# Performance work log

Measured on AMD Instinct MI355X. Metric: run time of the kernel, lower is better.

Reference implementation:

```python
import jax, jax.numpy as jnp
import numpy as np

N = 100000      # nodes
E = 1600000     # edges (avg degree 16)
F_IN = 128      # num_features
H = 128         # hidden_channels
OUT = 64        # out_channels


def _glorot(key, shape):
    lim = float(np.sqrt(6.0 / (shape[0] + shape[1])))
    return jax.random.uniform(key, shape, jnp.float32, -lim, lim)


def setup_inputs() -> dict:
    key = jax.random.key(0)
    ks = jax.random.split(key, 5)
    x = jax.random.normal(ks[0], (N, F_IN), jnp.float32)
    edge_index = jax.random.randint(ks[1], (2, E), 0, N, dtype=jnp.int64)
    W1 = _glorot(ks[2], (F_IN, H)); b1 = jnp.zeros((H,), jnp.float32)
    W2 = _glorot(ks[3], (H, H));    b2 = jnp.zeros((H,), jnp.float32)
    W3 = _glorot(ks[4], (H, OUT));  b3 = jnp.zeros((OUT,), jnp.float32)
    return {"x": x, "edge_index": edge_index,
            "W1": W1, "b1": b1, "W2": W2, "b2": b2, "W3": W3, "b3": b3}


def _gcn_conv(h, src, dst, norm, W, b, n):
    # PyG GCNConv: linear transform, then sym-normalized scatter aggregation, then bias
    h = h @ W                                   # [N, d_out]
    msg = h[src] * norm[:, None]                # gather + scale, [E+N, d_out]
    agg = jax.ops.segment_sum(msg, dst, num_segments=n)
    return agg + b


def reference(x, edge_index, W1, b1, W2, b2, W3, b3):
    n = x.shape[0]
    # add self-loops (GCNConv default add_self_loops=True)
    loop = jnp.arange(n, dtype=edge_index.dtype)
    src = jnp.concatenate([edge_index[0], loop])
    dst = jnp.concatenate([edge_index[1], loop])
    # symmetric normalization deg^-1/2[src] * deg^-1/2[dst]
    deg = jax.ops.segment_sum(jnp.ones_like(dst, x.dtype), dst, num_segments=n)
    dinv = jnp.where(deg > 0, jax.lax.rsqrt(deg), 0.0)
    norm = dinv[src] * dinv[dst]

    h = jax.nn.relu(_gcn_conv(x, src, dst, norm, W1, b1, n))  # dropout p=0 -> no-op
    h = jax.nn.relu(_gcn_conv(h, src, dst, norm, W2, b2, n))
    h = _gcn_conv(h, src, dst, norm, W3, b3, n)
    return jax.nn.log_softmax(h, axis=1)
```

## Files before the change

kernel.cpp:

```cpp
#include <hip/hip_runtime.h>
#include <stdint.h>
#include <math.h>

#define FIN 128

typedef __attribute__((ext_vector_type(8))) short short8v;
typedef __attribute__((ext_vector_type(4))) float float4v;
typedef __attribute__((ext_vector_type(2))) float float2v;

__device__ __forceinline__ uint32_t f2_to_bf2(float x, float y) {
    uint32_t r;
    asm("v_cvt_pk_bf16_f32 %0, %1, %2" : "=v"(r) : "v"(x), "v"(y));
    return r;
}
__device__ __forceinline__ unsigned short f_to_bf(float x) {
    union { float f; uint32_t i; } a;
    a.f = x;
    uint32_t u = a.i + 0x7FFF + ((a.i >> 16) & 1);
    return (unsigned short)(u >> 16);
}
__device__ __forceinline__ void acc16_fp8_pk(float2v* acc2, uint4 v) {
    uint32_t us[4] = {v.x, v.y, v.z, v.w};
#pragma unroll
    for (int q = 0; q < 4; ++q) {
        acc2[q * 2 + 0] += __builtin_amdgcn_cvt_pk_f32_fp8(us[q], false);
        acc2[q * 2 + 1] += __builtin_amdgcn_cvt_pk_f32_fp8(us[q], true);
    }
}

template <int CTRL>
__device__ __forceinline__ float dppmov(float x) {
    int i = __builtin_bit_cast(int, x);
    int r = __builtin_amdgcn_update_dpp(i, i, CTRL, 0xF, 0xF, false);
    return __builtin_bit_cast(float, r);
}
__device__ __forceinline__ float swz16f(float x) {
    int r = __builtin_amdgcn_ds_swizzle(__builtin_bit_cast(int, x), 0x401F);
    return __builtin_bit_cast(float, r);
}

__device__ __forceinline__ int edge_at(const void* ei, long long idx, int is32) {
    return is32 ? ((const int*)ei)[idx] : (int)((const long long*)ei)[idx];
}

#define SP_CHUNK 4096
__global__ __launch_bounds__(256) void splitA_kernel(
        const void* __restrict__ ei, int* __restrict__ gCnt,
        uint32_t* __restrict__ buf1, int E, int capS, int nA,
        const float* __restrict__ W1, const float* __restrict__ W2,
        const float* __restrict__ W3, unsigned short* __restrict__ Wf1,
        unsigned short* __restrict__ Wf2, unsigned short* __restrict__ Wf3) {
    __shared__ int hist[16];
    __shared__ int gbase[16];
    __shared__ int lflag;
    int t = threadIdx.x;
    if (blockIdx.x >= nA) {
        int idx = (blockIdx.x - nA) * 256 + t;
        const float* W;
        unsigned short* Wf;
        int NCOL, base;
        if (idx < 2048)      { W = W1; Wf = Wf1; NCOL = 128; base = idx; }
        else if (idx < 4096) { W = W2; Wf = Wf2; NCOL = 128; base = idx - 2048; }
        else if (idx < 5120) { W = W3; Wf = Wf3; NCOL = 64;  base = idx - 4096; }
        else return;
        int f = base >> 6, l = base & 63;
        int ct = f >> 2, ks = f & 3;
        int nn = ct * 16 + (l & 15);
        int k0 = ks * 32 + (l >> 4) * 8;
        uint32_t pk[4];
#pragma unroll
        for (int j = 0; j < 4; ++j) {
            float a = W[(size_t)(k0 + 2 * j) * NCOL + nn];
            float b = W[(size_t)(k0 + 2 * j + 1) * NCOL + nn];
            pk[j] = f2_to_bf2(a, b);
        }
        ((uint4*)Wf)[base] = make_uint4(pk[0], pk[1], pk[2], pk[3]);
        return;
    }
    if (t < 16) hist[t] = 0;
    if (t == 0) lflag = 0;
    long long base = (long long)blockIdx.x * SP_CHUNK;
    __syncthreads();
    {
        long long e = base + t;
        if (e < E && ((const int*)ei)[2 * e + 1] != 0) atomicOr(&lflag, 1);
    }
    __syncthreads();
    int is32 = lflag;
    uint32_t lrec[16], rec[16];
#pragma unroll
    for (int j = 0; j < 16; ++j) {
        long long e = base + t + j * 256;
        if (e < E) {
            int s = edge_at(ei, e, is32);
            int d = edge_at(ei, (long long)E + e, is32);
            int b = d >> 13;
            int lofs = atomicAdd(&hist[b], 1);
            lrec[j] = ((uint32_t)lofs << 4) | (uint32_t)b;
            rec[j] = ((uint32_t)s << 13) | (uint32_t)(d & 8191);
        } else
            lrec[j] = 0xFFFFFFFFu;
    }
    __syncthreads();
    if (t < 16) gbase[t] = atomicAdd(&gCnt[t], hist[t]);
    __syncthreads();
#pragma unroll
    for (int j = 0; j < 16; ++j) {
        if (lrec[j] != 0xFFFFFFFFu) {
            int b = lrec[j] & 15;
            int pos = gbase[b] + (int)(lrec[j] >> 4);
            if (pos < capS) buf1[(size_t)b * capS + pos] = rec[j];
        }
    }
}

__global__ __launch_bounds__(256) void splitB_kernel(const int* __restrict__ gCnt,
                                                     const uint32_t* __restrict__ buf1,
                                                     int* __restrict__ cnt2,
                                                     uint32_t* __restrict__ buf2,
                                                     int capS, int cap2, int NB) {
    __shared__ int hist[128];
    __shared__ int sbase[128];
    __shared__ int gbase[128];
    __shared__ uint32_t ordrec[SP_CHUNK];
    __shared__ unsigned char ordsub[SP_CHUNK];
    int t = threadIdx.x;
    int s = blockIdx.y;
    if (t < 128) hist[t] = 0;
    __syncthreads();
    int m = gCnt[s];
    if (m > capS) m = capS;
    long long base = (long long)blockIdx.x * SP_CHUNK;
    uint32_t lrec[16], r32[16];
#pragma unroll
    for (int j = 0; j < 16; ++j) {
        long long i = base + t + j * 256;
        if (i < m) {
            uint32_t r = buf1[(size_t)s * capS + i];
            int d13 = (int)(r & 8191u);
            int sub = d13 >> 6;
            int lofs = atomicAdd(&hist[sub], 1);
            lrec[j] = ((uint32_t)lofs << 7) | (uint32_t)sub;
            r32[j] = ((r >> 13) << 6) | (uint32_t)(d13 & 63);
        } else
            lrec[j] = 0xFFFFFFFFu;
    }
    __syncthreads();
    if (t < 128) sbase[t] = hist[t];
    __syncthreads();
    for (int off = 1; off < 128; off <<= 1) {
        int v = 0;
        if (t < 128 && t >= off) v = sbase[t - off];
        __syncthreads();
        if (t < 128) sbase[t] += v;
        __syncthreads();
    }
    if (t < 128) {
        int g = s * 128 + t;
        gbase[t] = (g < NB && hist[t] > 0) ? atomicAdd(&cnt2[g], hist[t]) : 0;
        sbase[t] -= hist[t];
    }
    __syncthreads();
#pragma unroll
    for (int j = 0; j < 16; ++j) {
        if (lrec[j] != 0xFFFFFFFFu) {
            int sub = lrec[j] & 127;
            int pos = sbase[sub] + (int)(lrec[j] >> 7);
            ordrec[pos] = r32[j];
            ordsub[pos] = (unsigned char)sub;
        }
    }
    __syncthreads();
    int mloc = (int)(m - base);
    if (mloc > SP_CHUNK) mloc = SP_CHUNK;
    if (mloc < 0) mloc = 0;
    for (int i = t; i < mloc; i += 256) {
        int sub = ordsub[i];
        int gpos = gbase[sub] + (i - sbase[sub]);
        if (gpos < cap2) buf2[(size_t)(s * 128 + sub) * cap2 + gpos] = ordrec[i];
    }
}

__global__ __launch_bounds__(256) void binBC_kernel(const int* __restrict__ cnt2,
                                                    const uint32_t* __restrict__ buf2,
                                                    int* __restrict__ cnt,
                                                    float* __restrict__ dinv,
                                                    int* __restrict__ rowstart,
                                                    int* __restrict__ col,
                                                    int n, int cap2) {
    __shared__ int h[64];
    __shared__ int rowst[64];
    __shared__ int cur[64];
    __shared__ int sc[64];
    int bin = blockIdx.x;
    int t = threadIdx.x;
    if (t < 64) {
        h[t] = (bin * 64 + t < n) ? 1 : 0;
        cur[t] = 1;
    }
    __syncthreads();
    int m = cnt2[bin];
    if (m > cap2) m = cap2;
    const uint32_t* buf = buf2 + (size_t)bin * cap2;
    for (int i = t; i < m; i += 256) atomicAdd(&h[buf[i] & 63], 1);
    __syncthreads();
    int c = 0, pc = 0;
    if (t < 64) { c = h[t]; pc = (c + 7) & ~7; sc[t] = pc; }
    __syncthreads();
    for (int off = 1; off < 64; off <<= 1) {
        int v = 0;
        if (t < 64 && t >= off) v = sc[t - off];
        __syncthreads();
        if (t < 64) sc[t] += v;
        __syncthreads();
    }
    if (t < 64) {
        int node = bin * 64 + t;
        int base = bin * cap2;
        int st = base + sc[t] - pc;
        rowst[t] = st;
        if (node < n) {
            cnt[node] = c;
            dinv[node] = rsqrtf((float)c);
            rowstart[node] = st;
            col[st] = node;
            for (int k = c; k < pc; ++k) col[st + k] = n;
        }
    }
    __syncthreads();
    for (int i = t; i < m; i += 256) {
        uint32_t rec = buf[i];
        int d6 = rec & 63;
        int off = atomicAdd(&cur[d6], 1);
        col[rowst[d6] + off] = (int)(rec >> 6);
    }
}

template <int NCOL, int A_FP32, int OUT_FP8>
__global__ __launch_bounds__(256) void gemm_mfma(const void* __restrict__ Av,
                                                 const unsigned short* __restrict__ Wf,
                                                 const float* __restrict__ dinv,
                                                 void* __restrict__ Cv, int n) {
    __shared__ unsigned short lds[NCOL * 128];
    const int t = threadIdx.x;
    if (blockIdx.x == 0 && t < NCOL / 4)
        ((uint32_t*)Cv)[(size_t)n * (NCOL / 4) + t] = 0;
    for (int i = t; i < NCOL * 16; i += 256)
        ((uint4*)lds)[i] = ((const uint4*)Wf)[i];
    __syncthreads();

    const int wave = t >> 6, lane = t & 63;
    const int row0 = blockIdx.x * 64 + wave * 16;
    const int m = lane & 15, quad = lane >> 4;
    int arow = row0 + m;
    if (arow >= n) arow = n - 1;

    short8v a[4];
    if (A_FP32) {
        const float* A = (const float*)Av;
#pragma unroll
        for (int ks = 0; ks < 4; ++ks) {
            float4 lo = *(const float4*)(A + (size_t)arow * 128 + ks * 32 + quad * 8);
            float4 hi = *(const float4*)(A + (size_t)arow * 128 + ks * 32 + quad * 8 + 4);
            union { short8v v; uint32_t u[4]; } pk;
            pk.u[0] = f2_to_bf2(lo.x, lo.y);
            pk.u[1] = f2_to_bf2(lo.z, lo.w);
            pk.u[2] = f2_to_bf2(hi.x, hi.y);
            pk.u[3] = f2_to_bf2(hi.z, hi.w);
            a[ks] = pk.v;
        }
    } else {
        const unsigned short* A = (const unsigned short*)Av;
#pragma unroll
        for (int ks = 0; ks < 4; ++ks)
            a[ks] = *(const short8v*)(A + (size_t)arow * 128 + ks * 32 + quad * 8);
    }

    const int cr0 = row0 + quad * 4;
    float ds[4];
#pragma unroll
    for (int r = 0; r < 4; ++r) {
        int gr = cr0 + r;
        ds[r] = (gr < n) ? dinv[gr] : 0.0f;
    }
#pragma unroll
    for (int ct = 0; ct < NCOL / 16; ++ct) {
        float4v acc = {0.0f, 0.0f, 0.0f, 0.0f};
#pragma unroll
        for (int ks = 0; ks < 4; ++ks) {
            int f = ct * 4 + ks;
            short8v b = *(const short8v*)(lds + ((size_t)(f * 64 + lane)) * 8);
            acc = __builtin_amdgcn_mfma_f32_16x16x32_bf16(a[ks], b, acc, 0, 0, 0);
        }
#pragma unroll
        for (int r = 0; r < 4; ++r) {
            int gr = cr0 + r;
            if (gr < n) {
                float val = acc[r] * ds[r];
                if (OUT_FP8) {
                    int u = __builtin_amdgcn_cvt_pk_fp8_f32(val, val, 0, false);
                    ((unsigned char*)Cv)[(size_t)gr * NCOL + ct * 16 + m] =
                        (unsigned char)(u & 0xFF);
                } else {
                    ((unsigned short*)Cv)[(size_t)gr * NCOL + ct * 16 + m] = f_to_bf(val);
                }
            }
        }
    }
}

__global__ __launch_bounds__(256) void agg_relu_128_fp8(
        const uint32_t* __restrict__ T8, const int* __restrict__ rowstart,
        const int* __restrict__ cnt, const int* __restrict__ col,
        const float* __restrict__ dinv, const float* __restrict__ bias,
        uint32_t* __restrict__ outHb, int n) {
    int wid = blockIdx.x * 4 + (threadIdx.x >> 6);
    int lane = threadIdx.x & 63;
    int j = lane & 7, slot = (lane >> 3) & 3, sel = lane >> 5;
    int nodeA = wid * 2;
    int node = nodeA + sel;
    if (nodeA >= n) return;
    bool valid = node < n;
    int nd = valid ? node : nodeA;
    int start = rowstart[nd];
    int c = cnt[nd];
    int nit = valid ? (((c + 7) & ~7) >> 3) : 0;

    float2v acc2[8];
#pragma unroll
    for (int k = 0; k < 8; ++k) acc2[k] = (float2v){0.0f, 0.0f};
    const uint4* T4 = (const uint4*)T8;
    int bp = start + slot;
    int s00 = col[bp +  0], s01 = col[bp +  4];
    int s10 = col[bp +  8], s11 = col[bp + 12];
    int s20 = col[bp + 16], s21 = col[bp + 20];
    int s30 = col[bp + 24], s31 = col[bp + 28];
    s00 = (0 < nit) ? s00 : n;  s01 = (0 < nit) ? s01 : n;
    s10 = (1 < nit) ? s10 : n;  s11 = (1 < nit) ? s11 : n;
    s20 = (2 < nit) ? s20 : n;  s21 = (2 < nit) ? s21 : n;
    s30 = (3 < nit) ? s30 : n;  s31 = (3 < nit) ? s31 : n;
    uint4 v00 = T4[(size_t)s00 * 8 + j], v01 = T4[(size_t)s01 * 8 + j];
    uint4 v10 = T4[(size_t)s10 * 8 + j], v11 = T4[(size_t)s11 * 8 + j];
    uint4 v20 = T4[(size_t)s20 * 8 + j], v21 = T4[(size_t)s21 * 8 + j];
    uint4 v30 = T4[(size_t)s30 * 8 + j], v31 = T4[(size_t)s31 * 8 + j];
    acc16_fp8_pk(acc2, v00); acc16_fp8_pk(acc2, v01);
    acc16_fp8_pk(acc2, v10); acc16_fp8_pk(acc2, v11);
    acc16_fp8_pk(acc2, v20); acc16_fp8_pk(acc2, v21);
    acc16_fp8_pk(acc2, v30); acc16_fp8_pk(acc2, v31);
    for (int s = 4; s < nit; ++s) {
        int a0 = col[bp + s * 8], a1 = col[bp + s * 8 + 4];
        uint4 w0 = T4[(size_t)a0 * 8 + j];
        uint4 w1 = T4[(size_t)a1 * 8 + j];
        acc16_fp8_pk(acc2, w0);
        acc16_fp8_pk(acc2, w1);
    }
    float* acc = (float*)acc2;
#pragma unroll
    for (int k = 0; k < 16; ++k) acc[k] += dppmov<0x128>(acc[k]);
#pragma unroll
    for (int k = 0; k < 16; ++k) acc[k] += swz16f(acc[k]);
    if (slot == 0 && valid) {
        float di = dinv[node];
        const float4* b4 = (const float4*)bias;
        float r[16];
#pragma unroll
        for (int q = 0; q < 4; ++q) {
            float4 bb = b4[j * 4 + q];
            r[q * 4 + 0] = fmaxf(di * acc[q * 4 + 0] + bb.x, 0.0f);
            r[q * 4 + 1] = fmaxf(di * acc[q * 4 + 1] + bb.y, 0.0f);
            r[q * 4 + 2] = fmaxf(di * acc[q * 4 + 2] + bb.z, 0.0f);
            r[q * 4 + 3] = fmaxf(di * acc[q * 4 + 3] + bb.w, 0.0f);
        }
        uint4 o0, o1;
        o0.x = f2_to_bf2(r[0], r[1]);   o0.y = f2_to_bf2(r[2], r[3]);
        o0.z = f2_to_bf2(r[4], r[5]);   o0.w = f2_to_bf2(r[6], r[7]);
        o1.x = f2_to_bf2(r[8], r[9]);   o1.y = f2_to_bf2(r[10], r[11]);
        o1.z = f2_to_bf2(r[12], r[13]); o1.w = f2_to_bf2(r[14], r[15]);
        *(uint4*)(outHb + (size_t)node * 64 + j * 8) = o0;
        *(uint4*)(outHb + (size_t)node * 64 + j * 8 + 4) = o1;
    }
}

__global__ __launch_bounds__(256) void agg_lsm_64_fp8(
        const uint32_t* __restrict__ T8, const int* __restrict__ rowstart,
        const int* __restrict__ cnt, const int* __restrict__ col,
        const float* __restrict__ dinv, const float* __restrict__ bias,
        float* __restrict__ out, int n) {
    int wid = blockIdx.x * 4 + (threadIdx.x >> 6);
    int lane = threadIdx.x & 63;
    int j = lane & 3, slot = (lane >> 2) & 7, sel = lane >> 5;
    int nodeA = wid * 2;
    int node = nodeA + sel;
    if (nodeA >= n) return;
    bool valid = node < n;
    int nd = valid ? node : nodeA;
    int start = rowstart[nd];
    int c = cnt[nd];
    int nit = valid ? (((c + 7) & ~7) >> 3) : 0;

    float2v acc2[8];
#pragma unroll
    for (int k = 0; k < 8; ++k) acc2[k] = (float2v){0.0f, 0.0f};
    const uint4* T4 = (const uint4*)T8;
    int bp = start + slot;
    int a0 = col[bp +  0];
    int a1 = col[bp +  8];
    int a2 = col[bp + 16];
    int a3 = col[bp + 24];
    a0 = (0 < nit) ? a0 : n;
    a1 = (1 < nit) ? a1 : n;
    a2 = (2 < nit) ? a2 : n;
    a3 = (3 < nit) ? a3 : n;
    uint4 v0 = T4[(size_t)a0 * 4 + j];
    uint4 v1 = T4[(size_t)a1 * 4 + j];
    uint4 v2 = T4[(size_t)a2 * 4 + j];
    uint4 v3 = T4[(size_t)a3 * 4 + j];
    acc16_fp8_pk(acc2, v0);
    acc16_fp8_pk(acc2, v1);
    acc16_fp8_pk(acc2, v2);
    acc16_fp8_pk(acc2, v3);
    for (int s = 4; s < nit; ++s) {
        int aa = col[bp + s * 8];
        uint4 w = T4[(size_t)aa * 4 + j];
        acc16_fp8_pk(acc2, w);
    }
    float* acc = (float*)acc2;
#pragma unroll
    for (int k = 0; k < 16; ++k) acc[k] += dppmov<0x124>(acc[k]);
#pragma unroll
    for (int k = 0; k < 16; ++k) acc[k] += dppmov<0x128>(acc[k]);
#pragma unroll
    for (int k = 0; k < 16; ++k) acc[k] += swz16f(acc[k]);
    float di = dinv[nd];
    const float4* b4 = (const float4*)bias;
    float r[16];
#pragma unroll
    for (int q = 0; q < 4; ++q) {
        float4 bb = b4[j * 4 + q];
        r[q * 4 + 0] = di * acc[q * 4 + 0] + bb.x;
        r[q * 4 + 1] = di * acc[q * 4 + 1] + bb.y;
        r[q * 4 + 2] = di * acc[q * 4 + 2] + bb.z;
        r[q * 4 + 3] = di * acc[q * 4 + 3] + bb.w;
    }
    float m0 = fmaxf(fmaxf(r[0], r[1]), fmaxf(r[2], r[3]));
    float m1 = fmaxf(fmaxf(r[4], r[5]), fmaxf(r[6], r[7]));
    float m2 = fmaxf(fmaxf(r[8], r[9]), fmaxf(r[10], r[11]));
    float m3 = fmaxf(fmaxf(r[12], r[13]), fmaxf(r[14], r[15]));
    float m = fmaxf(fmaxf(m0, m1), fmaxf(m2, m3));
    m = fmaxf(m, dppmov<0xB1>(m));
    m = fmaxf(m, dppmov<0x4E>(m));
    float e0 = __expf(r[0] - m) + __expf(r[1] - m) + __expf(r[2] - m) +
               __expf(r[3] - m);
    float e1 = __expf(r[4] - m) + __expf(r[5] - m) + __expf(r[6] - m) +
               __expf(r[7] - m);
    float e2 = __expf(r[8] - m) + __expf(r[9] - m) + __expf(r[10] - m) +
               __expf(r[11] - m);
    float e3 = __expf(r[12] - m) + __expf(r[13] - m) + __expf(r[14] - m) +
               __expf(r[15] - m);
    float ss = (e0 + e1) + (e2 + e3);
    ss += dppmov<0xB1>(ss);
    ss += dppmov<0x4E>(ss);
    float lg = m + __logf(ss);
    if (slot == 0 && valid) {
#pragma unroll
        for (int q = 0; q < 4; ++q) {
            float4 o = make_float4(r[q * 4 + 0] - lg, r[q * 4 + 1] - lg,
                                   r[q * 4 + 2] - lg, r[q * 4 + 3] - lg);
            *(float4*)(out + (size_t)node * 64 + j * 16 + q * 4) = o;
        }
    }
}

extern "C" void kernel_launch(void* const* d_in, const int* in_sizes, int n_in,
                              void* d_out, int out_size, void* d_ws, size_t ws_size,
                              hipStream_t stream) {
    const float* x  = (const float*)d_in[0];
    const void*  ei = d_in[1];
    const float* W1 = (const float*)d_in[2];
    const float* b1 = (const float*)d_in[3];
    const float* W2 = (const float*)d_in[4];
    const float* b2 = (const float*)d_in[5];
    const float* W3 = (const float*)d_in[6];
    const float* b3 = (const float*)d_in[7];
    float* out = (float*)d_out;

    const int n = in_sizes[0] / FIN;
    const int E = in_sizes[1] / 2;

    char* p = (char*)d_ws;
    auto carve = [&](size_t bytes) {
        char* q = p;
        p += (bytes + 255) & ~(size_t)255;
        return q;
    };
    const int NB = (n + 63) / 64;
    const int NS = (n + 8191) / 8192;

    long long meanS = (long long)E * 8192 / n;
    int capS = (int)(meanS + 8 * (long long)sqrt((double)meanS) + 1024);
    capS = (capS + 15) & ~15;
    long long mean2 = (long long)E * 64 / n;
    int cap2 = (int)(mean2 + 8 * (long long)sqrt((double)mean2) + 1152);
    cap2 = (cap2 + 15) & ~15;

    int*   cnt      = (int*)carve((size_t)n * 4);
    int*   rowstart = (int*)carve((size_t)n * 4);
    float* dinv     = (float*)carve((size_t)n * 4);
    int*   colb     = (int*)carve(((size_t)NB * cap2 + 4096) * 4);
    int*   gCnt     = (int*)carve((size_t)(16 + NB) * 4);
    int*   cnt2     = gCnt + 16;
    size_t Tbytes = (size_t)n * 128 + 256;
    size_t Hbytes = (size_t)n * 128 * 2;
    char*  TH = carve(Tbytes + Hbytes);
    void*  T  = (void*)TH;
    unsigned short* Hb = (unsigned short*)(TH + Tbytes);
    unsigned short* Wf1 = (unsigned short*)carve(128 * 128 * 2);
    unsigned short* Wf2 = (unsigned short*)carve(128 * 128 * 2);
    unsigned short* Wf3 = (unsigned short*)carve(128 * 64 * 2);

    size_t buf1B = ((size_t)NS * capS * 4 + 255) & ~(size_t)255;
    uint32_t* buf1 = (uint32_t*)TH;
    uint32_t* buf2 = (uint32_t*)(TH + buf1B);
    size_t avail2 = (Tbytes + Hbytes > buf1B) ? (Tbytes + Hbytes - buf1B) : 0;
    size_t maxc2 = avail2 / ((size_t)NB * 4);
    if ((size_t)cap2 > maxc2) cap2 = (int)maxc2;

    hipMemsetAsync(gCnt, 0, (size_t)(16 + NB) * 4, stream);

    const int gagg2 = ((n + 1) / 2 + 3) / 4;
    const int ggemm = (n + 63) / 64;
    const int gsplitA = (E + SP_CHUNK - 1) / SP_CHUNK;
    const int gsplitBx = (capS + SP_CHUNK - 1) / SP_CHUNK;

    splitA_kernel<<<gsplitA + 20, 256, 0, stream>>>(ei, gCnt, buf1, E, capS, gsplitA,
                                                    W1, W2, W3, Wf1, Wf2, Wf3);
    splitB_kernel<<<dim3(gsplitBx, NS), 256, 0, stream>>>(gCnt, buf1, cnt2, buf2, capS,
                                                          cap2, NB);
    binBC_kernel<<<NB, 256, 0, stream>>>(cnt2, buf2, cnt, dinv, rowstart, colb, n,
                                         cap2);

    gemm_mfma<128, 1, 1><<<ggemm, 256, 0, stream>>>(x, Wf1, dinv, T, n);
    agg_relu_128_fp8<<<gagg2, 256, 0, stream>>>((const uint32_t*)T, rowstart, cnt,
                                                colb, dinv, b1, (uint32_t*)Hb, n);
    gemm_mfma<128, 0, 1><<<ggemm, 256, 0, stream>>>(Hb, Wf2, dinv, T, n);
    agg_relu_128_fp8<<<gagg2, 256, 0, stream>>>((const uint32_t*)T, rowstart, cnt,
                                                colb, dinv, b2, (uint32_t*)Hb, n);
    gemm_mfma<64, 0, 1><<<ggemm, 256, 0, stream>>>(Hb, Wf3, dinv, T, n);
    agg_lsm_64_fp8<<<gagg2, 256, 0, stream>>>((const uint32_t*)T, rowstart, cnt, colb,
                                              dinv, b3, out, n);
}
```

Measured before the change: 278.3 us.

## Split 128-wide aggregation into four feature slices processed by separate blocks

The 128-feature FP8 aggregation kernel now splits each node's feature row into four 32-byte slices. Blocks are interleaved so neighbouring blocks handle different slices of the same node pairs, and each lane gathers 8 bytes instead of 16. The lane layout moves to 4 feature lanes by 8 edge slots, with an extra DPP reduction step. The aim is to shrink the working set per wave and raise memory-level parallelism. The cost is four times as many blocks, each re-reading col indices and rowstart/cnt, plus smaller gather transactions.

```diff
diff --git a/kernel.cpp b/kernel.cpp
--- a/kernel.cpp
+++ b/kernel.cpp
@@ -26,6 +26,12 @@
         acc2[q * 2 + 0] += __builtin_amdgcn_cvt_pk_f32_fp8(us[q], false);
         acc2[q * 2 + 1] += __builtin_amdgcn_cvt_pk_f32_fp8(us[q], true);
     }
+}
+__device__ __forceinline__ void acc8_fp8_pk(float2v* acc2, uint2 v) {
+    acc2[0] += __builtin_amdgcn_cvt_pk_f32_fp8(v.x, false);
+    acc2[1] += __builtin_amdgcn_cvt_pk_f32_fp8(v.x, true);
+    acc2[2] += __builtin_amdgcn_cvt_pk_f32_fp8(v.y, false);
+    acc2[3] += __builtin_amdgcn_cvt_pk_f32_fp8(v.y, true);
 }
 
 template <int CTRL>
@@ -314,9 +320,12 @@
         const int* __restrict__ cnt, const int* __restrict__ col,
         const float* __restrict__ dinv, const float* __restrict__ bias,
         uint32_t* __restrict__ outHb, int n) {
-    int wid = blockIdx.x * 4 + (threadIdx.x >> 6);
+    int b = blockIdx.x;
+    int slice = (b >> 1) & 3;
+    int p = (b >> 3) * 2 + (b & 1);
+    int wid = p * 4 + (threadIdx.x >> 6);
     int lane = threadIdx.x & 63;
-    int j = lane & 7, slot = (lane >> 3) & 3, sel = lane >> 5;
+    int j = lane & 3, slot = (lane >> 2) & 7, sel = lane >> 5;
     int nodeA = wid * 2;
     int node = nodeA + sel;
     if (nodeA >= n) return;
@@ -326,58 +335,60 @@
     int c = cnt[nd];
     int nit = valid ? (((c + 7) & ~7) >> 3) : 0;
 
-    float2v acc2[8];
-#pragma unroll
-    for (int k = 0; k < 8; ++k) acc2[k] = (float2v){0.0f, 0.0f};
-    const uint4* T4 = (const uint4*)T8;
+    float2v acc2[4];
+#pragma unroll
+    for (int k = 0; k < 4; ++k) acc2[k] = (float2v){0.0f, 0.0f};
+    const uint2* T2 = (const uint2*)T8;
     int bp = start + slot;
-    int s00 = col[bp +  0], s01 = col[bp +  4];
-    int s10 = col[bp +  8], s11 = col[bp + 12];
-    int s20 = col[bp + 16], s21 = col[bp + 20];
-    int s30 = col[bp + 24], s31 = col[bp + 28];
-    s00 = (0 < nit) ? s00 : n;  s01 = (0 < nit) ? s01 : n;
-    s10 = (1 < nit) ? s10 : n;  s11 = (1 < nit) ? s11 : n;
-    s20 = (2 < nit) ? s20 : n;  s21 = (2 < nit) ? s21 : n;
-    s30 = (3 < nit) ? s30 : n;  s31 = (3 < nit) ? s31 : n;
-    uint4 v00 = T4[(size_t)s00 * 8 + j], v01 = T4[(size_t)s01 * 8 + j];
-    uint4 v10 = T4[(size_t)s10 * 8 + j], v11 = T4[(size_t)s11 * 8 + j];
-    uint4 v20 = T4[(size_t)s20 * 8 + j], v21 = T4[(size_t)s21 * 8 + j];
-    uint4 v30 = T4[(size_t)s30 * 8 + j], v31 = T4[(size_t)s31 * 8 + j];
-    acc16_fp8_pk(acc2, v00); acc16_fp8_pk(acc2, v01);
-    acc16_fp8_pk(acc2, v10); acc16_fp8_pk(acc2, v11);
-    acc16_fp8_pk(acc2, v20); acc16_fp8_pk(acc2, v21);
-    acc16_fp8_pk(acc2, v30); acc16_fp8_pk(acc2, v31);
+    int fo = slice * 4 + j;
+    int a0 = col[bp +  0];
+    int a1 = col[bp +  8];
+    int a2 = col[bp + 16];
+    int a3 = col[bp + 24];
+    a0 = (0 < nit) ? a0 : n;
+    a1 = (1 < nit) ? a1 : n;
+    a2 = (2 < nit) ? a2 : n;
+    a3 = (3 < nit) ? a3 : n;
+    uint2 v0 = T2[(size_t)a0 * 16 + fo];
+    uint2 v1 = T2[(size_t)a1 * 16 + fo];
+    uint2 v2 = T2[(size_t)a2 * 16 + fo];
+    uint2 v3 = T2[(size_t)a3 * 16 + fo];
+    acc8_fp8_pk(acc2, v0);
+    acc8_fp8_pk(acc2, v1);
+    acc8_fp8_pk(acc2, v2);
+    acc8_fp8_pk(acc2, v3);
     for (int s = 4; s < nit; ++s) {
-        int a0 = col[bp + s * 8], a1 = col[bp + s * 8 + 4];
-        uint4 w0 = T4[(size_t)a0 * 8 + j];
-        uint4 w1 = T4[(size_t)a1 * 8 + j];
-        acc16_fp8_pk(acc2, w0);
-        acc16_fp8_pk(acc2, w1);
+        int aa = col[bp + s * 8];
+        uint2 w = T2[(size_t)aa * 16 + fo];
+        acc8_fp8_pk(acc2, w);
     }
     float* acc = (float*)acc2;
 #pragma unroll
-    for (int k = 0; k < 16; ++k) acc[k] += dppmov<0x128>(acc[k]);
-#pragma unroll
-    for (int k = 0; k < 16; ++k) acc[k] += swz16f(acc[k]);
+    for (int k = 0; k < 8; ++k) acc[k] += dppmov<0x124>(acc[k]);
+#pragma unroll
+    for (int k = 0; k < 8; ++k) acc[k] += dppmov<0x128>(acc[k]);
+#pragma unroll
+    for (int k = 0; k < 8; ++k) acc[k] += swz16f(acc[k]);
     if (slot == 0 && valid) {
         float di = dinv[node];
         const float4* b4 = (const float4*)bias;
-        float r[16];
-#pragma unroll
-        for (int q = 0; q < 4; ++q) {
-            float4 bb = b4[j * 4 + q];
-            r[q * 4 + 0] = fmaxf(di * acc[q * 4 + 0] + bb.x, 0.0f);
-            r[q * 4 + 1] = fmaxf(di * acc[q * 4 + 1] + bb.y, 0.0f);
-            r[q * 4 + 2] = fmaxf(di * acc[q * 4 + 2] + bb.z, 0.0f);
-            r[q * 4 + 3] = fmaxf(di * acc[q * 4 + 3] + bb.w, 0.0f);
-        }
-        uint4 o0, o1;
-        o0.x = f2_to_bf2(r[0], r[1]);   o0.y = f2_to_bf2(r[2], r[3]);
-        o0.z = f2_to_bf2(r[4], r[5]);   o0.w = f2_to_bf2(r[6], r[7]);
-        o1.x = f2_to_bf2(r[8], r[9]);   o1.y = f2_to_bf2(r[10], r[11]);
-        o1.z = f2_to_bf2(r[12], r[13]); o1.w = f2_to_bf2(r[14], r[15]);
-        *(uint4*)(outHb + (size_t)node * 64 + j * 8) = o0;
-        *(uint4*)(outHb + (size_t)node * 64 + j * 8 + 4) = o1;
+        float4 bb0 = b4[slice * 8 + j * 2];
+        float4 bb1 = b4[slice * 8 + j * 2 + 1];
+        float r[8];
+        r[0] = fmaxf(di * acc[0] + bb0.x, 0.0f);
+        r[1] = fmaxf(di * acc[1] + bb0.y, 0.0f);
+        r[2] = fmaxf(di * acc[2] + bb0.z, 0.0f);
+        r[3] = fmaxf(di * acc[3] + bb0.w, 0.0f);
+        r[4] = fmaxf(di * acc[4] + bb1.x, 0.0f);
+        r[5] = fmaxf(di * acc[5] + bb1.y, 0.0f);
+        r[6] = fmaxf(di * acc[6] + bb1.z, 0.0f);
+        r[7] = fmaxf(di * acc[7] + bb1.w, 0.0f);
+        uint4 o;
+        o.x = f2_to_bf2(r[0], r[1]);
+        o.y = f2_to_bf2(r[2], r[3]);
+        o.z = f2_to_bf2(r[4], r[5]);
+        o.w = f2_to_bf2(r[6], r[7]);
+        *(uint4*)(outHb + (size_t)node * 64 + slice * 16 + j * 4) = o;
     }
 }
 
@@ -528,6 +539,7 @@
     hipMemsetAsync(gCnt, 0, (size_t)(16 + NB) * 4, stream);
 
     const int gagg2 = ((n + 1) / 2 + 3) / 4;
+    const int gaggS = ((gagg2 + 1) / 2) * 8;
     const int ggemm = (n + 63) / 64;
     const int gsplitA = (E + SP_CHUNK - 1) / SP_CHUNK;
     const int gsplitBx = (capS + SP_CHUNK - 1) / SP_CHUNK;
@@ -540,10 +552,10 @@
                                          cap2);
 
     gemm_mfma<128, 1, 1><<<ggemm, 256, 0, stream>>>(x, Wf1, dinv, T, n);
-    agg_relu_128_fp8<<<gagg2, 256, 0, stream>>>((const uint32_t*)T, rowstart, cnt,
+    agg_relu_128_fp8<<<gaggS, 256, 0, stream>>>((const uint32_t*)T, rowstart, cnt,
                                                 colb, dinv, b1, (uint32_t*)Hb, n);
     gemm_mfma<128, 0, 1><<<ggemm, 256, 0, stream>>>(Hb, Wf2, dinv, T, n);
-    agg_relu_128_fp8<<<gagg2, 256, 0, stream>>>((const uint32_t*)T, rowstart, cnt,
+    agg_relu_128_fp8<<<gaggS, 256, 0, stream>>>((const uint32_t*)T, rowstart, cnt,
                                                 colb, dinv, b2, (uint32_t*)Hb, n);
     gemm_mfma<64, 0, 1><<<ggemm, 256, 0, stream>>>(Hb, Wf3, dinv, T, n);
     agg_lsm_64_fp8<<<gagg2, 256, 0, stream>>>((const uint32_t*)T, rowstart, cnt, colb,
```

Result: slower. 409.7 us (+47.2%).
